# Kernel tuning notes

Hardware: AMD Instinct MI355X
Metric: run time of the kernel (lower is better)

Reference implementation:

```python
import jax, jax.numpy as jnp
import numpy as np

SQRT_D = 8.0

def setup_inputs() -> dict:
    key = jax.random.key(0)
    kq, kk, kv = jax.random.split(key, 3)
    shape = (2, 16, 2048, 64)  # [batch, heads, seq, head_dim]
    return {
        "q": jax.random.normal(kq, shape, dtype=jnp.float32),
        "k": jax.random.normal(kk, shape, dtype=jnp.float32),
        "v": jax.random.normal(kv, shape, dtype=jnp.float32),
    }

def reference(q, k, v):
    # score = softmax(QK^T / sqrt_d) over the key axis j
    scores = jnp.einsum('bhif,bhjf->bhij', q, k) / SQRT_D
    probs = jax.nn.softmax(scores, axis=-1)
    # Note: original returns output permuted to [b, i, h, f]
    attn = jnp.einsum('bhij,bhjf->bihf', probs, v)
    return attn
```

## Files before the change

kernel.cpp:

```cpp
#include <hip/hip_runtime.h>

#define S_LEN 2048
#define HEADS 16
#define DIM 64

typedef __attribute__((ext_vector_type(8))) short short8;
typedef __attribute__((ext_vector_type(16))) float float16v;
typedef __attribute__((ext_vector_type(4))) float float4v;
typedef __attribute__((ext_vector_type(4))) unsigned uint4v;

static __device__ __forceinline__ unsigned pkbf(float lo, float hi) {
  unsigned r;
  asm("v_cvt_pk_bf16_f32 %0, %1, %2" : "=v"(r) : "v"(lo), "v"(hi));
  return r;
}

__global__ __launch_bounds__(256) void prep(const float* __restrict__ kk,
                                            const float* __restrict__ vv,
                                            short* __restrict__ kb,
                                            short* __restrict__ vt) {
  __shared__ unsigned t32[64 * 33];
  const int bx = blockIdx.x;
  const int bh = bx >> 5;
  const int j0 = (bx & 31) * 64;
  const int tid = threadIdx.x;

  {
    const int j = tid >> 2, f0 = (tid & 3) * 16;
    const float4v* src = (const float4v*)(kk + ((size_t)bh * S_LEN + j0 + j) * DIM + f0);
    float4v a0 = src[0], a1 = src[1], a2 = src[2], a3 = src[3];
    uint4v w0, w1;
    w0[0] = pkbf(a0[0], a0[1]); w0[1] = pkbf(a0[2], a0[3]);
    w0[2] = pkbf(a1[0], a1[1]); w0[3] = pkbf(a1[2], a1[3]);
    w1[0] = pkbf(a2[0], a2[1]); w1[1] = pkbf(a2[2], a2[3]);
    w1[2] = pkbf(a3[0], a3[1]); w1[3] = pkbf(a3[2], a3[3]);
    short* dstb = kb + (size_t)bh * (S_LEN * DIM) +
                  ((j0 >> 5) + (j >> 5)) * 2048 + (f0 >> 4) * 512 + (j & 31) * 8;
    *(uint4v*)dstb = w0;
    *(uint4v*)(dstb + 256) = w1;
  }
  {
    const int jp = (tid & 31) * 2, f0 = (tid >> 5) * 8;
    const int pp = ((jp & ~12) | ((jp & 4) << 1) | ((jp & 8) >> 1)) >> 1;
    const float* r0 = vv + ((size_t)bh * S_LEN + j0 + jp) * DIM + f0;
    const float* r1 = r0 + DIM;
    float4v a0 = *(const float4v*)r0, a1 = *(const float4v*)(r0 + 4);
    float4v b0 = *(const float4v*)r1, b1 = *(const float4v*)(r1 + 4);
#pragma unroll
    for (int e = 0; e < 4; e++) {
      t32[(f0 + e) * 33 + pp]     = pkbf(a0[e], b0[e]);
      t32[(f0 + 4 + e) * 33 + pp] = pkbf(a1[e], b1[e]);
    }
  }
  __syncthreads();
  {
    const int f = tid >> 2, x0 = (tid & 3) * 8;
    uint4v c0 = *(const uint4v*)&t32[f * 33 + x0];
    uint4v c1 = *(const uint4v*)&t32[f * 33 + x0 + 4];
    const int jt = (j0 >> 5) + (x0 >> 4);
    const int qd = (f >> 5) * 2 + ((x0 >> 3) & 1);
    short* dstb = vt + (size_t)bh * (S_LEN * DIM) + jt * 2048 + qd * 512 + (f & 31) * 8;
    *(uint4v*)dstb = c0;
    *(uint4v*)(dstb + 256) = c1;
  }
}

__global__ __launch_bounds__(128, 2) void attn_fwd(const float* __restrict__ q,
                                                   const short* __restrict__ kb,
                                                   const short* __restrict__ vt,
                                                   float* __restrict__ out) {
  __shared__ alignas(16) float smem[8704];
  const int bx0 = blockIdx.x;
  const int bx = (bx0 & 7) * 128 + (bx0 >> 3);
  const int bh = bx >> 5, it = bx & 31;
  const int b = bh >> 4, h = bh & 15;
  const int tid = threadIdx.x;
  const int w = tid >> 6, lane = tid & 63;
  const int n = lane & 31, hf = lane >> 5;
  const int i0 = it * 64;

  short8 qa0[4], qa1[4];
  {
    const float sc = 0.125f * 1.44269504088896f;
    const float* qr = q + ((size_t)bh * S_LEN + i0 + n) * DIM + hf * 8;
#pragma unroll
    for (int ks = 0; ks < 4; ks++) {
      float4v x0 = *(const float4v*)(qr + ks * 16);
      float4v x1 = *(const float4v*)(qr + ks * 16 + 4);
      uint4v pk_;
      pk_[0] = pkbf(x0[0] * sc, x0[1] * sc); pk_[1] = pkbf(x0[2] * sc, x0[3] * sc);
      pk_[2] = pkbf(x1[0] * sc, x1[1] * sc); pk_[3] = pkbf(x1[2] * sc, x1[3] * sc);
      qa0[ks] = *(short8*)&pk_;
      float4v y0 = *(const float4v*)(qr + 32 * DIM + ks * 16);
      float4v y1 = *(const float4v*)(qr + 32 * DIM + ks * 16 + 4);
      pk_[0] = pkbf(y0[0] * sc, y0[1] * sc); pk_[1] = pkbf(y0[2] * sc, y0[3] * sc);
      pk_[2] = pkbf(y1[0] * sc, y1[1] * sc); pk_[3] = pkbf(y1[2] * sc, y1[3] * sc);
      qa1[ks] = *(short8*)&pk_;
    }
  }

  const short* kp = kb + (size_t)bh * (S_LEN * DIM) + (size_t)w * (S_LEN * DIM / 2) + lane * 8;
  const short* vp = vt + (size_t)bh * (S_LEN * DIM) + (size_t)w * (S_LEN * DIM / 2) + lane * 8;

  short8 kf[4], vf[4];
#pragma unroll
  for (int u = 0; u < 4; u++) {
    kf[u] = *(const short8*)(kp + u * 512);
    vf[u] = *(const short8*)(vp + u * 512);
  }

  float16v zz;
#pragma unroll
  for (int e = 0; e < 16; e++) zz[e] = 0.f;
  float16v a00 = zz, a01 = zz, a10 = zz, a11 = zz;
  float lpa0 = 0.f, lpb0 = 0.f, lpa1 = 0.f, lpb1 = 0.f;

#pragma unroll 1
  for (int t = 0; t < 32; ++t) {
    const int adv = (t < 31) ? 2048 : 0;
    __builtin_amdgcn_s_setprio(1);
    float16v st0 = __builtin_amdgcn_mfma_f32_32x32x16_bf16(kf[0], qa0[0], zz, 0, 0, 0);
    float16v st1 = __builtin_amdgcn_mfma_f32_32x32x16_bf16(kf[0], qa1[0], zz, 0, 0, 0);
#pragma unroll
    for (int ks = 1; ks < 4; ks++) {
      st0 = __builtin_amdgcn_mfma_f32_32x32x16_bf16(kf[ks], qa0[ks], st0, 0, 0, 0);
      st1 = __builtin_amdgcn_mfma_f32_32x32x16_bf16(kf[ks], qa1[ks], st1, 0, 0, 0);
    }
    __builtin_amdgcn_s_setprio(0);
    kp += adv;
#pragma unroll
    for (int u = 0; u < 4; u++) kf[u] = *(const short8*)(kp + u * 512);

#pragma unroll
    for (int e = 0; e < 16; e++) {
      st0[e] = __builtin_amdgcn_exp2f(st0[e]);
      st1[e] = __builtin_amdgcn_exp2f(st1[e]);
    }
#pragma unroll
    for (int e = 0; e < 8; e++) {
      lpa0 += st0[2 * e]; lpb0 += st0[2 * e + 1];
      lpa1 += st1[2 * e]; lpb1 += st1[2 * e + 1];
    }
    uint4v pb00, pb01, pb10, pb11;
#pragma unroll
    for (int u = 0; u < 4; u++) {
      pb00[u] = pkbf(st0[2 * u], st0[2 * u + 1]);
      pb01[u] = pkbf(st0[8 + 2 * u], st0[8 + 2 * u + 1]);
      pb10[u] = pkbf(st1[2 * u], st1[2 * u + 1]);
      pb11[u] = pkbf(st1[8 + 2 * u], st1[8 + 2 * u + 1]);
    }
    short8 p00 = *(short8*)&pb00, p01 = *(short8*)&pb01;
    short8 p10 = *(short8*)&pb10, p11 = *(short8*)&pb11;

    __builtin_amdgcn_s_setprio(1);
    a00 = __builtin_amdgcn_mfma_f32_32x32x16_bf16(vf[0], p00, a00, 0, 0, 0);
    a00 = __builtin_amdgcn_mfma_f32_32x32x16_bf16(vf[1], p01, a00, 0, 0, 0);
    a01 = __builtin_amdgcn_mfma_f32_32x32x16_bf16(vf[0], p10, a01, 0, 0, 0);
    a01 = __builtin_amdgcn_mfma_f32_32x32x16_bf16(vf[1], p11, a01, 0, 0, 0);
    a10 = __builtin_amdgcn_mfma_f32_32x32x16_bf16(vf[2], p00, a10, 0, 0, 0);
    a10 = __builtin_amdgcn_mfma_f32_32x32x16_bf16(vf[3], p01, a10, 0, 0, 0);
    a11 = __builtin_amdgcn_mfma_f32_32x32x16_bf16(vf[2], p10, a11, 0, 0, 0);
    a11 = __builtin_amdgcn_mfma_f32_32x32x16_bf16(vf[3], p11, a11, 0, 0, 0);
    __builtin_amdgcn_s_setprio(0);
    vp += adv;
#pragma unroll
    for (int u = 0; u < 4; u++) vf[u] = *(const short8*)(vp + u * 512);
  }

  float d0 = lpa0 + lpb0;
  float d1 = lpa1 + lpb1;
  d0 += __shfl_xor(d0, 32);
  d1 += __shfl_xor(d1, 32);

  float* const ob = smem;
  float* const xb = smem + 4352;
  float* const db = smem + 8448;

  {
    float16v sA = w ? a00 : a10;
    float16v sB = w ? a01 : a11;
#pragma unroll
    for (int c = 0; c < 4; c++) {
      float4v u0, u1;
#pragma unroll
      for (int e = 0; e < 4; e++) { u0[e] = sA[4 * c + e]; u1[e] = sB[4 * c + e]; }
      *(float4v*)&xb[w * 2048 + c * 256 + lane * 4] = u0;
      *(float4v*)&xb[w * 2048 + 1024 + c * 256 + lane * 4] = u1;
    }
    db[w * 128 + lane] = d0;
    db[w * 128 + 64 + lane] = d1;
  }
  __syncthreads();
  {
    const int ow = 1 - w;
    float16v mA = w ? a10 : a00;
    float16v mB = w ? a11 : a01;
    const float iv0 = 1.f / (d0 + db[ow * 128 + lane]);
    const float iv1 = 1.f / (d1 + db[ow * 128 + 64 + lane]);
#pragma unroll
    for (int c = 0; c < 4; c++) {
      float4v u0 = *(const float4v*)&xb[ow * 2048 + c * 256 + lane * 4];
      float4v u1 = *(const float4v*)&xb[ow * 2048 + 1024 + c * 256 + lane * 4];
      float4v t0, t1;
#pragma unroll
      for (int e = 0; e < 4; e++) {
        t0[e] = (mA[4 * c + e] + u0[e]) * iv0;
        t1[e] = (mB[4 * c + e] + u1[e]) * iv1;
      }
      *(float4v*)&ob[n * 68 + w * 32 + 8 * c + 4 * hf] = t0;
      *(float4v*)&ob[(32 + n) * 68 + w * 32 + 8 * c + 4 * hf] = t1;
    }
  }
  __syncthreads();
  {
    const int il = tid >> 1, fq = (tid & 1) * 32;
    const float* src = &ob[il * 68 + fq];
    float* dst = out + (((size_t)b * S_LEN + i0 + il) * HEADS + h) * DIM + fq;
#pragma unroll
    for (int u = 0; u < 8; u++) ((float4v*)dst)[u] = ((const float4v*)src)[u];
  }
}

extern "C" void kernel_launch(void* const* d_in, const int* in_sizes, int n_in,
                              void* d_out, int out_size, void* d_ws, size_t ws_size,
                              hipStream_t stream) {
  const float* q = (const float*)d_in[0];
  const float* k = (const float*)d_in[1];
  const float* v = (const float*)d_in[2];
  float* out = (float*)d_out;
  short* kb = (short*)d_ws;
  short* vt = (short*)d_ws + (size_t)32 * S_LEN * DIM;

  prep<<<1024, 256, 0, stream>>>(k, v, kb, vt);
  attn_fwd<<<1024, 128, 0, stream>>>(q, kb, vt, out);
}
```

Measured before the change: 134.6 us.

## Split the key/value sequence across four waves per block with a ring reduction

Each block now runs four waves instead of two, and each wave covers a quarter of the key/value sequence, so the main loop runs 16 iterations instead of 32. Partial accumulators and softmax denominators are then combined through a rotating LDS-slot exchange with barriers, and each wave normalizes and writes one 32x32 quadrant of the output. The aim is more waves in flight and shorter per-wave loops to hide memory and MFMA latency. The cost is three rounds of LDS exchange plus barriers, and a tighter register budget under launch bounds of 256 threads and 4 blocks, which may cause spilling. It also uses float4 LDS accesses at a stride of 33 floats, which are not 16-byte aligned.

```diff
diff --git a/kernel.cpp b/kernel.cpp
--- a/kernel.cpp
+++ b/kernel.cpp
@@ -65,11 +65,11 @@
   }
 }
 
-__global__ __launch_bounds__(128, 2) void attn_fwd(const float* __restrict__ q,
+__global__ __launch_bounds__(256, 4) void attn_fwd(const float* __restrict__ q,
                                                    const short* __restrict__ kb,
                                                    const short* __restrict__ vt,
                                                    float* __restrict__ out) {
-  __shared__ alignas(16) float smem[8704];
+  __shared__ alignas(16) float smem[4 * 1056 + 256];
   const int bx0 = blockIdx.x;
   const int bx = (bx0 & 7) * 128 + (bx0 >> 3);
   const int bh = bx >> 5, it = bx & 31;
@@ -99,8 +99,8 @@
     }
   }
 
-  const short* kp = kb + (size_t)bh * (S_LEN * DIM) + (size_t)w * (S_LEN * DIM / 2) + lane * 8;
-  const short* vp = vt + (size_t)bh * (S_LEN * DIM) + (size_t)w * (S_LEN * DIM / 2) + lane * 8;
+  const short* kp = kb + (size_t)bh * (S_LEN * DIM) + (size_t)w * (S_LEN * DIM / 4) + lane * 8;
+  const short* vp = vt + (size_t)bh * (S_LEN * DIM) + (size_t)w * (S_LEN * DIM / 4) + lane * 8;
 
   short8 kf[4], vf[4];
 #pragma unroll
@@ -116,8 +116,8 @@
   float lpa0 = 0.f, lpb0 = 0.f, lpa1 = 0.f, lpb1 = 0.f;
 
 #pragma unroll 1
-  for (int t = 0; t < 32; ++t) {
-    const int adv = (t < 31) ? 2048 : 0;
+  for (int t = 0; t < 16; ++t) {
+    const int adv = (t < 15) ? 2048 : 0;
     __builtin_amdgcn_s_setprio(1);
     float16v st0 = __builtin_amdgcn_mfma_f32_32x32x16_bf16(kf[0], qa0[0], zz, 0, 0, 0);
     float16v st1 = __builtin_amdgcn_mfma_f32_32x32x16_bf16(kf[0], qa1[0], zz, 0, 0, 0);
@@ -172,52 +172,55 @@
   d0 += __shfl_xor(d0, 32);
   d1 += __shfl_xor(d1, 32);
 
-  float* const ob = smem;
-  float* const xb = smem + 4352;
-  float* const db = smem + 8448;
-
-  {
-    float16v sA = w ? a00 : a10;
-    float16v sB = w ? a01 : a11;
+  float* const slots = smem;
+  float* const db = smem + 4 * 1056;
+
+  if (hf == 0) { db[w * 64 + n] = d0; db[w * 64 + 32 + n] = d1; }
+
+  float16v own = (w == 0) ? a00 : (w == 1) ? a10 : (w == 2) ? a01 : a11;
+#pragma unroll
+  for (int r = 1; r < 4; r++) {
+    const int s = (w + r) & 3;
+    float16v snd = (s == 0) ? a00 : (s == 1) ? a10 : (s == 2) ? a01 : a11;
+    float* sl = slots + w * 1056;
 #pragma unroll
     for (int c = 0; c < 4; c++) {
-      float4v u0, u1;
-#pragma unroll
-      for (int e = 0; e < 4; e++) { u0[e] = sA[4 * c + e]; u1[e] = sB[4 * c + e]; }
-      *(float4v*)&xb[w * 2048 + c * 256 + lane * 4] = u0;
-      *(float4v*)&xb[w * 2048 + 1024 + c * 256 + lane * 4] = u1;
-    }
-    db[w * 128 + lane] = d0;
-    db[w * 128 + 64 + lane] = d1;
-  }
-  __syncthreads();
-  {
-    const int ow = 1 - w;
-    float16v mA = w ? a10 : a00;
-    float16v mB = w ? a11 : a01;
-    const float iv0 = 1.f / (d0 + db[ow * 128 + lane]);
-    const float iv1 = 1.f / (d1 + db[ow * 128 + 64 + lane]);
+      float4v u;
+#pragma unroll
+      for (int e = 0; e < 4; e++) u[e] = snd[4 * c + e];
+      *(float4v*)&sl[c * 256 + lane * 4] = u;
+    }
+    __syncthreads();
+    const float* rl = slots + ((w - r) & 3) * 1056;
 #pragma unroll
     for (int c = 0; c < 4; c++) {
-      float4v u0 = *(const float4v*)&xb[ow * 2048 + c * 256 + lane * 4];
-      float4v u1 = *(const float4v*)&xb[ow * 2048 + 1024 + c * 256 + lane * 4];
-      float4v t0, t1;
-#pragma unroll
-      for (int e = 0; e < 4; e++) {
-        t0[e] = (mA[4 * c + e] + u0[e]) * iv0;
-        t1[e] = (mB[4 * c + e] + u1[e]) * iv1;
-      }
-      *(float4v*)&ob[n * 68 + w * 32 + 8 * c + 4 * hf] = t0;
-      *(float4v*)&ob[(32 + n) * 68 + w * 32 + 8 * c + 4 * hf] = t1;
-    }
-  }
-  __syncthreads();
-  {
-    const int il = tid >> 1, fq = (tid & 1) * 32;
-    const float* src = &ob[il * 68 + fq];
-    float* dst = out + (((size_t)b * S_LEN + i0 + il) * HEADS + h) * DIM + fq;
-#pragma unroll
-    for (int u = 0; u < 8; u++) ((float4v*)dst)[u] = ((const float4v*)src)[u];
+      float4v u = *(const float4v*)&rl[c * 256 + lane * 4];
+#pragma unroll
+      for (int e = 0; e < 4; e++) own[4 * c + e] += u[e];
+    }
+    __syncthreads();
+  }
+
+  const int myit = w >> 1;
+  const float dt = db[myit * 32 + n] + db[64 + myit * 32 + n] +
+                   db[128 + myit * 32 + n] + db[192 + myit * 32 + n];
+  const float inv = 1.f / dt;
+
+  float* const tb = slots + w * 1056;
+#pragma unroll
+  for (int c = 0; c < 4; c++) {
+    float4v u;
+#pragma unroll
+    for (int e = 0; e < 4; e++) u[e] = own[4 * c + e] * inv;
+    *(float4v*)&tb[n * 33 + 8 * c + 4 * hf] = u;
+  }
+  {
+    const int il = lane >> 1, fq2 = (lane & 1) * 16;
+    const float* src = &tb[il * 33 + fq2];
+    float* dst = out + (((size_t)b * S_LEN + i0 + myit * 32 + il) * HEADS + h) * DIM +
+                 (w & 1) * 32 + fq2;
+#pragma unroll
+    for (int u = 0; u < 4; u++) ((float4v*)dst)[u] = ((const float4v*)src)[u];
   }
 }
 
@@ -232,5 +235,5 @@
   short* vt = (short*)d_ws + (size_t)32 * S_LEN * DIM;
 
   prep<<<1024, 256, 0, stream>>>(k, v, kb, vt);
-  attn_fwd<<<1024, 128, 0, stream>>>(q, kb, vt, out);
-}
+  attn_fwd<<<1024, 256, 0, stream>>>(q, kb, vt, out);
+}
```

After: 401.4 us. 198% more time.

## Serialize the two S-tile chains to cut registers and shrink the epilogue LDS

Applied to the files above, without the earlier changes.

The main loop now computes the first score tile's MFMA chain, exp2, sum and bf16 pack before starting the second tile's chain, so fewer score registers are live at once. Launch bounds move from 2 to 3 blocks per SIMD. The epilogue reduction is reorganized so each wave normalizes one query half and writes its own output rows, which shrinks shared memory from 8704 to 4480 floats. This should raise occupancy, at the cost of less MFMA/exp overlap within a wave and a possible risk of register spills.

```diff
diff --git a/kernel.cpp b/kernel.cpp
--- a/kernel.cpp
+++ b/kernel.cpp
@@ -65,11 +65,11 @@
   }
 }
 
-__global__ __launch_bounds__(128, 2) void attn_fwd(const float* __restrict__ q,
+__global__ __launch_bounds__(128, 3) void attn_fwd(const float* __restrict__ q,
                                                    const short* __restrict__ kb,
                                                    const short* __restrict__ vt,
                                                    float* __restrict__ out) {
-  __shared__ alignas(16) float smem[8704];
+  __shared__ alignas(16) float smem[4480];
   const int bx0 = blockIdx.x;
   const int bx = (bx0 & 7) * 128 + (bx0 >> 3);
   const int bh = bx >> 5, it = bx & 31;
@@ -120,32 +120,38 @@
     const int adv = (t < 31) ? 2048 : 0;
     __builtin_amdgcn_s_setprio(1);
     float16v st0 = __builtin_amdgcn_mfma_f32_32x32x16_bf16(kf[0], qa0[0], zz, 0, 0, 0);
-    float16v st1 = __builtin_amdgcn_mfma_f32_32x32x16_bf16(kf[0], qa1[0], zz, 0, 0, 0);
-#pragma unroll
-    for (int ks = 1; ks < 4; ks++) {
+#pragma unroll
+    for (int ks = 1; ks < 4; ks++)
       st0 = __builtin_amdgcn_mfma_f32_32x32x16_bf16(kf[ks], qa0[ks], st0, 0, 0, 0);
-      st1 = __builtin_amdgcn_mfma_f32_32x32x16_bf16(kf[ks], qa1[ks], st1, 0, 0, 0);
-    }
     __builtin_amdgcn_s_setprio(0);
-    kp += adv;
-#pragma unroll
-    for (int u = 0; u < 4; u++) kf[u] = *(const short8*)(kp + u * 512);
-
-#pragma unroll
-    for (int e = 0; e < 16; e++) {
-      st0[e] = __builtin_amdgcn_exp2f(st0[e]);
-      st1[e] = __builtin_amdgcn_exp2f(st1[e]);
-    }
-#pragma unroll
-    for (int e = 0; e < 8; e++) {
-      lpa0 += st0[2 * e]; lpb0 += st0[2 * e + 1];
-      lpa1 += st1[2 * e]; lpb1 += st1[2 * e + 1];
-    }
-    uint4v pb00, pb01, pb10, pb11;
+#pragma unroll
+    for (int e = 0; e < 16; e++) st0[e] = __builtin_amdgcn_exp2f(st0[e]);
+#pragma unroll
+    for (int e = 0; e < 8; e++) { lpa0 += st0[2 * e]; lpb0 += st0[2 * e + 1]; }
+    uint4v pb00, pb01;
 #pragma unroll
     for (int u = 0; u < 4; u++) {
       pb00[u] = pkbf(st0[2 * u], st0[2 * u + 1]);
       pb01[u] = pkbf(st0[8 + 2 * u], st0[8 + 2 * u + 1]);
+    }
+
+    __builtin_amdgcn_s_setprio(1);
+    float16v st1 = __builtin_amdgcn_mfma_f32_32x32x16_bf16(kf[0], qa1[0], zz, 0, 0, 0);
+#pragma unroll
+    for (int ks = 1; ks < 4; ks++)
+      st1 = __builtin_amdgcn_mfma_f32_32x32x16_bf16(kf[ks], qa1[ks], st1, 0, 0, 0);
+    __builtin_amdgcn_s_setprio(0);
+    kp += adv;
+#pragma unroll
+    for (int u = 0; u < 4; u++) kf[u] = *(const short8*)(kp + u * 512);
+
+#pragma unroll
+    for (int e = 0; e < 16; e++) st1[e] = __builtin_amdgcn_exp2f(st1[e]);
+#pragma unroll
+    for (int e = 0; e < 8; e++) { lpa1 += st1[2 * e]; lpb1 += st1[2 * e + 1]; }
+    uint4v pb10, pb11;
+#pragma unroll
+    for (int u = 0; u < 4; u++) {
       pb10[u] = pkbf(st1[2 * u], st1[2 * u + 1]);
       pb11[u] = pkbf(st1[8 + 2 * u], st1[8 + 2 * u + 1]);
     }
@@ -172,50 +178,56 @@
   d0 += __shfl_xor(d0, 32);
   d1 += __shfl_xor(d1, 32);
 
-  float* const ob = smem;
-  float* const xb = smem + 4352;
-  float* const db = smem + 8448;
-
-  {
-    float16v sA = w ? a00 : a10;
-    float16v sB = w ? a01 : a11;
+  float* const db = smem + 4352;
+  if (hf == 0) { db[w * 64 + n] = d0; db[w * 64 + 32 + n] = d1; }
+
+  {
+    float* buf = smem + (1 - w) * 2176;
+    float16v s0 = w ? a00 : a01;
+    float16v s1 = w ? a10 : a11;
 #pragma unroll
     for (int c = 0; c < 4; c++) {
       float4v u0, u1;
 #pragma unroll
-      for (int e = 0; e < 4; e++) { u0[e] = sA[4 * c + e]; u1[e] = sB[4 * c + e]; }
-      *(float4v*)&xb[w * 2048 + c * 256 + lane * 4] = u0;
-      *(float4v*)&xb[w * 2048 + 1024 + c * 256 + lane * 4] = u1;
-    }
-    db[w * 128 + lane] = d0;
-    db[w * 128 + 64 + lane] = d1;
+      for (int e = 0; e < 4; e++) { u0[e] = s0[4 * c + e]; u1[e] = s1[4 * c + e]; }
+      *(float4v*)&buf[c * 256 + lane * 4] = u0;
+      *(float4v*)&buf[1024 + c * 256 + lane * 4] = u1;
+    }
   }
   __syncthreads();
-  {
-    const int ow = 1 - w;
-    float16v mA = w ? a10 : a00;
-    float16v mB = w ? a11 : a01;
-    const float iv0 = 1.f / (d0 + db[ow * 128 + lane]);
-    const float iv1 = 1.f / (d1 + db[ow * 128 + 64 + lane]);
+
+  float16v o0 = w ? a01 : a00;
+  float16v o1 = w ? a11 : a10;
+  {
+    const float dt = db[w * 32 + n] + db[64 + w * 32 + n];
+    const float inv = 1.f / dt;
+    const float* buf = smem + w * 2176;
 #pragma unroll
     for (int c = 0; c < 4; c++) {
-      float4v u0 = *(const float4v*)&xb[ow * 2048 + c * 256 + lane * 4];
-      float4v u1 = *(const float4v*)&xb[ow * 2048 + 1024 + c * 256 + lane * 4];
-      float4v t0, t1;
+      float4v u0 = *(const float4v*)&buf[c * 256 + lane * 4];
+      float4v u1 = *(const float4v*)&buf[1024 + c * 256 + lane * 4];
 #pragma unroll
       for (int e = 0; e < 4; e++) {
-        t0[e] = (mA[4 * c + e] + u0[e]) * iv0;
-        t1[e] = (mB[4 * c + e] + u1[e]) * iv1;
+        o0[4 * c + e] = (o0[4 * c + e] + u0[e]) * inv;
+        o1[4 * c + e] = (o1[4 * c + e] + u1[e]) * inv;
       }
-      *(float4v*)&ob[n * 68 + w * 32 + 8 * c + 4 * hf] = t0;
-      *(float4v*)&ob[(32 + n) * 68 + w * 32 + 8 * c + 4 * hf] = t1;
     }
   }
   __syncthreads();
-  {
-    const int il = tid >> 1, fq = (tid & 1) * 32;
-    const float* src = &ob[il * 68 + fq];
-    float* dst = out + (((size_t)b * S_LEN + i0 + il) * HEADS + h) * DIM + fq;
+
+  float* const tb = smem + w * 2176;
+#pragma unroll
+  for (int c = 0; c < 4; c++) {
+    float4v u0, u1;
+#pragma unroll
+    for (int e = 0; e < 4; e++) { u0[e] = o0[4 * c + e]; u1[e] = o1[4 * c + e]; }
+    *(float4v*)&tb[n * 68 + 8 * c + 4 * hf] = u0;
+    *(float4v*)&tb[n * 68 + 32 + 8 * c + 4 * hf] = u1;
+  }
+  {
+    const int il = lane >> 1, fq = (lane & 1) * 32;
+    const float* src = &tb[il * 68 + fq];
+    float* dst = out + (((size_t)b * S_LEN + i0 + w * 32 + il) * HEADS + h) * DIM + fq;
 #pragma unroll
     for (int u = 0; u < 8; u++) ((float4v*)dst)[u] = ((const float4v*)src)[u];
   }
```

Result: no change. 136.6 us (+1.5%).
